# Performance work log

Hardware: AMD Instinct MI355X
Metric: run time of the kernel (lower is better)

Reference implementation:

```python
import jax, jax.numpy as jnp
import numpy as np

PI = 3.14159265358979323846
MARGIN = 6.0
DIM = 256
ENT_TOT = 43234
REL_RANGE = (6.0 + 2.0) / DIM  # (margin + epsilon) / dim = 0.03125


def setup_inputs() -> dict:
    key = jax.random.key(0)
    k1, k2, k3 = jax.random.split(key, 3)
    head = jax.random.normal(k1, (32, 2 * DIM), dtype=jnp.float32)
    relation = jax.random.normal(k2, (32, DIM), dtype=jnp.float32)
    ent_emb = jax.random.normal(k3, (ENT_TOT, 2 * DIM), dtype=jnp.float32)
    return {"head": head, "relation": relation, "ent_emb": ent_emb}


def reference(head, relation, ent_emb):
    # head: (B, 2D) -> re/im halves (B, D)
    re_h, im_h = jnp.split(head, 2, axis=-1)
    # entity table: (E, 2D) -> (E, D) each
    re_t, im_t = jnp.split(ent_emb, 2, axis=-1)
    # phase rotation from relation embedding
    phase = relation / (REL_RANGE / PI)          # (B, D)
    re_r = jnp.cos(phase)
    im_r = jnp.sin(phase)
    # complex rotation of head by relation: (B, D)
    re_rot = re_h * re_r - im_h * im_r
    im_rot = re_h * im_r + im_h * re_r
    # difference against every entity, broadcast to (B, E, D)
    re_s = re_rot[:, None, :] - re_t[None, :, :]
    im_s = im_rot[:, None, :] - im_t[None, :, :]
    # L2 norm over the complex pair, summed over D -> (B, E)
    dist = jnp.sqrt(re_s * re_s + im_s * im_s).sum(axis=-1)
    return MARGIN - dist
```

## Files before the change

kernel.cpp:

```cpp
#include <hip/hip_runtime.h>
#include <math.h>

#define DIMH 256
#define NB   32
#define E_TOT 43234
#define TE   64
#define DK   32
#define DQ   128
#define NC   (DQ / DK)
#define PHASE_DIV 0.009947183943243459f

typedef float v2f __attribute__((ext_vector_type(2)));
typedef float v4f __attribute__((ext_vector_type(4)));

__global__ __launch_bounds__(256) void init_kernel(float* __restrict__ out) {
    int i = blockIdx.x * 256 + threadIdx.x;
    if (i < (NB * E_TOT) / 4) {
        float4 v = make_float4(6.0f, 6.0f, 6.0f, 6.0f);
        reinterpret_cast<float4*>(out)[i] = v;
    }
}

__global__ void rot_kernel(const float* __restrict__ head,
                           const float* __restrict__ rel,
                           float* __restrict__ rot) {
    int i = blockIdx.x * blockDim.x + threadIdx.x;
    int b = i >> 8;
    int d = i & 255;
    float re_h = head[b * 2 * DIMH + d];
    float im_h = head[b * 2 * DIMH + DIMH + d];
    float ph = rel[b * DIMH + d] / PHASE_DIV;
    float s, c;
    sincosf(ph, &s, &c);
    rot[b * DIMH + d]             = re_h * c - im_h * s;
    rot[NB * DIMH + b * DIMH + d] = re_h * s + im_h * c;
}

__device__ __forceinline__ v2f sqrt2(v2f s) {
    v2f r;
    r.x = __builtin_amdgcn_sqrtf(s.x);
    r.y = __builtin_amdgcn_sqrtf(s.y);
    return r;
}

__global__ __launch_bounds__(256, 6) void dist_kernel(const float* __restrict__ ent,
                                                      const float* __restrict__ rot,
                                                      float* __restrict__ out) {
    __shared__ v4f s_e[TE][DK / 2 + 1];
    __shared__ v4f s_r[NB][DK / 2 + 1];

    const int tid   = threadIdx.x;
    const int etile = blockIdx.x >> 1;
    const int half  = blockIdx.x & 1;
    const int eb    = etile * TE;
    const int eg    = tid & 31;
    const int bg    = (tid >> 5) * 4;
    const int dbase = half * DQ;

    const int er0 = min(eb + (tid >> 3), E_TOT - 1);
    const int er1 = min(eb + ((tid + 256) >> 3), E_TOT - 1);
    const int ec0 = (tid & 7) << 2;
    const int rrow = tid >> 3;

    float4 pe_re[2], pe_im[2], p_rr, p_ri;

    auto load_chunk = [&](int dk) {
        const float* b0 = &ent[(size_t)er0 * (2 * DIMH)];
        const float* b1 = &ent[(size_t)er1 * (2 * DIMH)];
        pe_re[0] = *reinterpret_cast<const float4*>(b0 + dk + ec0);
        pe_im[0] = *reinterpret_cast<const float4*>(b0 + DIMH + dk + ec0);
        pe_re[1] = *reinterpret_cast<const float4*>(b1 + dk + ec0);
        pe_im[1] = *reinterpret_cast<const float4*>(b1 + DIMH + dk + ec0);
        p_rr = *reinterpret_cast<const float4*>(&rot[rrow * DIMH + dk + ec0]);
        p_ri = *reinterpret_cast<const float4*>(&rot[NB * DIMH + rrow * DIMH + dk + ec0]);
    };

    v2f acc[4][2];
    #pragma unroll
    for (int j = 0; j < 4; ++j)
        #pragma unroll
        for (int k = 0; k < 2; ++k) { acc[j][k].x = 0.f; acc[j][k].y = 0.f; }

    load_chunk(dbase);

    for (int c = 0; c < NC; ++c) {
        {
            int c4 = tid & 7;
            #pragma unroll
            for (int it = 0; it < 2; ++it) {
                int row = (tid + it * 256) >> 3;
                v4f lo, hi;
                lo.x = pe_re[it].x; lo.y = pe_re[it].y; lo.z = pe_im[it].x; lo.w = pe_im[it].y;
                hi.x = pe_re[it].z; hi.y = pe_re[it].w; hi.z = pe_im[it].z; hi.w = pe_im[it].w;
                s_e[row][2 * c4]     = lo;
                s_e[row][2 * c4 + 1] = hi;
            }
            v4f lo, hi;
            lo.x = p_rr.x; lo.y = p_rr.y; lo.z = p_ri.x; lo.w = p_ri.y;
            hi.x = p_rr.z; hi.y = p_rr.w; hi.z = p_ri.z; hi.w = p_ri.w;
            s_r[rrow][2 * c4]     = lo;
            s_r[rrow][2 * c4 + 1] = hi;
        }
        __syncthreads();

        if (c + 1 < NC) load_chunk(dbase + (c + 1) * DK);

        #pragma unroll 4
        for (int p = 0; p < DK / 2; ++p) {
            v4f r4[4], e4[2];
            #pragma unroll
            for (int j = 0; j < 4; ++j) r4[j] = s_r[bg + j][p];
            #pragma unroll
            for (int k = 0; k < 2; ++k) e4[k] = s_e[eg + 32 * k][p];
            #pragma unroll
            for (int j = 0; j < 4; ++j)
                #pragma unroll
                for (int k = 0; k < 2; ++k) {
                    v2f a = r4[j].xy - e4[k].xy;
                    v2f b = r4[j].zw - e4[k].zw;
                    v2f s = a * a + b * b;
                    acc[j][k] += sqrt2(s);
                }
        }
        __syncthreads();
    }

    #pragma unroll
    for (int k = 0; k < 2; ++k) {
        int e = eb + eg + 32 * k;
        if (e < E_TOT) {
            #pragma unroll
            for (int j = 0; j < 4; ++j)
                atomicAdd(&out[(size_t)(bg + j) * E_TOT + e],
                          -(acc[j][k].x + acc[j][k].y));
        }
    }
}

extern "C" void kernel_launch(void* const* d_in, const int* in_sizes, int n_in,
                              void* d_out, int out_size, void* d_ws, size_t ws_size,
                              hipStream_t stream) {
    const float* head = (const float*)d_in[0];
    const float* rel  = (const float*)d_in[1];
    const float* ent  = (const float*)d_in[2];
    float* rot = (float*)d_ws;

    int init_blocks = ((NB * E_TOT) / 4 + 255) / 256;
    init_kernel<<<init_blocks, 256, 0, stream>>>((float*)d_out);
    rot_kernel<<<(NB * DIMH) / 256, 256, 0, stream>>>(head, rel, rot);

    int etiles = (E_TOT + TE - 1) / TE;
    dist_kernel<<<etiles * 2, 256, 0, stream>>>(ent, rot, (float*)d_out);
}
```

Measured before the change: 209.7 us.

## Replace init+atomicAdd with partial-sum buffers and a reduce kernel

The output is no longer pre-filled with the margin and accumulated with atomics. Each half-dimension block now writes its partial sum to a workspace buffer, and a separate reduce kernel adds the two halves and subtracts from the margin. If the workspace is too small, a fallback runs a single pass over the full dimension and writes the output directly. This removes the atomic read-modify-write traffic and the init pass, but adds a 2x-size intermediate write and a read-back in the reduce kernel.

```diff
diff --git a/kernel.cpp b/kernel.cpp
--- a/kernel.cpp
+++ b/kernel.cpp
@@ -7,19 +7,10 @@
 #define TE   64
 #define DK   32
 #define DQ   128
-#define NC   (DQ / DK)
 #define PHASE_DIV 0.009947183943243459f
 
 typedef float v2f __attribute__((ext_vector_type(2)));
 typedef float v4f __attribute__((ext_vector_type(4)));
-
-__global__ __launch_bounds__(256) void init_kernel(float* __restrict__ out) {
-    int i = blockIdx.x * 256 + threadIdx.x;
-    if (i < (NB * E_TOT) / 4) {
-        float4 v = make_float4(6.0f, 6.0f, 6.0f, 6.0f);
-        reinterpret_cast<float4*>(out)[i] = v;
-    }
-}
 
 __global__ void rot_kernel(const float* __restrict__ head,
                            const float* __restrict__ rel,
@@ -43,15 +34,17 @@
     return r;
 }
 
+template<bool DIRECT>
 __global__ __launch_bounds__(256, 6) void dist_kernel(const float* __restrict__ ent,
                                                       const float* __restrict__ rot,
-                                                      float* __restrict__ out) {
+                                                      float* __restrict__ dst) {
     __shared__ v4f s_e[TE][DK / 2 + 1];
     __shared__ v4f s_r[NB][DK / 2 + 1];
 
     const int tid   = threadIdx.x;
-    const int etile = blockIdx.x >> 1;
-    const int half  = blockIdx.x & 1;
+    const int etile = DIRECT ? blockIdx.x : (blockIdx.x >> 1);
+    const int half  = DIRECT ? 0 : (blockIdx.x & 1);
+    const int NC    = DIRECT ? (DIMH / DK) : (DQ / DK);
     const int eb    = etile * TE;
     const int eg    = tid & 31;
     const int bg    = (tid >> 5) * 4;
@@ -130,10 +123,30 @@
         int e = eb + eg + 32 * k;
         if (e < E_TOT) {
             #pragma unroll
-            for (int j = 0; j < 4; ++j)
-                atomicAdd(&out[(size_t)(bg + j) * E_TOT + e],
-                          -(acc[j][k].x + acc[j][k].y));
+            for (int j = 0; j < 4; ++j) {
+                float s = acc[j][k].x + acc[j][k].y;
+                if (DIRECT) {
+                    dst[(size_t)(bg + j) * E_TOT + e] = 6.0f - s;
+                } else {
+                    dst[(size_t)half * (NB * E_TOT) + (size_t)(bg + j) * E_TOT + e] = s;
+                }
+            }
         }
+    }
+}
+
+__global__ __launch_bounds__(256) void reduce_kernel(const float* __restrict__ part,
+                                                     float* __restrict__ out) {
+    int i = blockIdx.x * 256 + threadIdx.x;
+    if (i < (NB * E_TOT) / 4) {
+        float4 a = reinterpret_cast<const float4*>(part)[i];
+        float4 b = reinterpret_cast<const float4*>(part + (size_t)NB * E_TOT)[i];
+        float4 o;
+        o.x = 6.0f - (a.x + b.x);
+        o.y = 6.0f - (a.y + b.y);
+        o.z = 6.0f - (a.z + b.z);
+        o.w = 6.0f - (a.w + b.w);
+        reinterpret_cast<float4*>(out)[i] = o;
     }
 }
 
@@ -143,12 +156,19 @@
     const float* head = (const float*)d_in[0];
     const float* rel  = (const float*)d_in[1];
     const float* ent  = (const float*)d_in[2];
-    float* rot = (float*)d_ws;
+    float* rot  = (float*)d_ws;
+    float* part = rot + 2 * NB * DIMH;
 
-    int init_blocks = ((NB * E_TOT) / 4 + 255) / 256;
-    init_kernel<<<init_blocks, 256, 0, stream>>>((float*)d_out);
     rot_kernel<<<(NB * DIMH) / 256, 256, 0, stream>>>(head, rel, rot);
 
-    int etiles = (E_TOT + TE - 1) / TE;
-    dist_kernel<<<etiles * 2, 256, 0, stream>>>(ent, rot, (float*)d_out);
+    const size_t need = (size_t)(2 * NB * DIMH) * 4 + (size_t)2 * NB * E_TOT * 4;
+    const int etiles = (E_TOT + TE - 1) / TE;
+
+    if (ws_size >= need) {
+        dist_kernel<false><<<etiles * 2, 256, 0, stream>>>(ent, rot, part);
+        int rblocks = ((NB * E_TOT) / 4 + 255) / 256;
+        reduce_kernel<<<rblocks, 256, 0, stream>>>(part, (float*)d_out);
+    } else {
+        dist_kernel<true><<<etiles, 256, 0, stream>>>(ent, rot, (float*)d_out);
+    }
 }
```

Measured after the change: 210.9 us. About the same (+0.6%).

## Store LDS tiles as bf16, drop D-split and atomics, remove init kernel

Applied to the files above, without the earlier changes.

Entity and rotated-head values are rounded to bf16 and packed into 8-byte words in shared memory, which halves LDS footprint and read traffic per inner iteration. Each block now covers the full D range instead of half, so the output is written directly with the margin applied. This removes the init kernel and the atomicAdd traffic. The cost is lower precision in the distance sum from the bf16 rounding, plus added pack and unpack ALU work and half as many blocks.

```diff
diff --git a/kernel.cpp b/kernel.cpp
--- a/kernel.cpp
+++ b/kernel.cpp
@@ -6,34 +6,53 @@
 #define E_TOT 43234
 #define TE   64
 #define DK   32
-#define DQ   128
-#define NC   (DQ / DK)
+#define NC   (DIMH / DK)
 #define PHASE_DIV 0.009947183943243459f
 
 typedef float v2f __attribute__((ext_vector_type(2)));
-typedef float v4f __attribute__((ext_vector_type(4)));
 
-__global__ __launch_bounds__(256) void init_kernel(float* __restrict__ out) {
-    int i = blockIdx.x * 256 + threadIdx.x;
-    if (i < (NB * E_TOT) / 4) {
-        float4 v = make_float4(6.0f, 6.0f, 6.0f, 6.0f);
-        reinterpret_cast<float4*>(out)[i] = v;
-    }
+__device__ __forceinline__ unsigned bf16_rne(float f) {
+    unsigned u = __float_as_uint(f);
+    return (u + 0x7FFFu + ((u >> 16) & 1u)) >> 16;
+}
+__device__ __forceinline__ unsigned pack_bf16(float f0, float f1) {
+    return bf16_rne(f0) | (bf16_rne(f1) << 16);
+}
+__device__ __forceinline__ v2f unpack_bf16(unsigned w) {
+    v2f r;
+    r.x = __uint_as_float(w << 16);
+    r.y = __uint_as_float(w & 0xFFFF0000u);
+    return r;
 }
 
-__global__ void rot_kernel(const float* __restrict__ head,
-                           const float* __restrict__ rel,
-                           float* __restrict__ rot) {
-    int i = blockIdx.x * blockDim.x + threadIdx.x;
-    int b = i >> 8;
-    int d = i & 255;
-    float re_h = head[b * 2 * DIMH + d];
-    float im_h = head[b * 2 * DIMH + DIMH + d];
-    float ph = rel[b * DIMH + d] / PHASE_DIV;
-    float s, c;
-    sincosf(ph, &s, &c);
-    rot[b * DIMH + d]             = re_h * c - im_h * s;
-    rot[NB * DIMH + b * DIMH + d] = re_h * s + im_h * c;
+__global__ __launch_bounds__(256) void rot_kernel(const float* __restrict__ head,
+                                                  const float* __restrict__ rel,
+                                                  uint2* __restrict__ rot_bf) {
+    int i  = blockIdx.x * 256 + threadIdx.x;
+    int b  = i >> 7;
+    int dp = i & 127;
+    int d0 = dp * 2;
+    float re0, re1, im0, im1;
+    {
+        float re_h = head[b * 2 * DIMH + d0];
+        float im_h = head[b * 2 * DIMH + DIMH + d0];
+        float s, c;
+        sincosf(rel[b * DIMH + d0] / PHASE_DIV, &s, &c);
+        re0 = re_h * c - im_h * s;
+        im0 = re_h * s + im_h * c;
+    }
+    {
+        float re_h = head[b * 2 * DIMH + d0 + 1];
+        float im_h = head[b * 2 * DIMH + DIMH + d0 + 1];
+        float s, c;
+        sincosf(rel[b * DIMH + d0 + 1] / PHASE_DIV, &s, &c);
+        re1 = re_h * c - im_h * s;
+        im1 = re_h * s + im_h * c;
+    }
+    uint2 w;
+    w.x = pack_bf16(re0, re1);
+    w.y = pack_bf16(im0, im1);
+    rot_bf[b * (DIMH / 2) + dp] = w;
 }
 
 __device__ __forceinline__ v2f sqrt2(v2f s) {
@@ -43,36 +62,39 @@
     return r;
 }
 
-__global__ __launch_bounds__(256, 6) void dist_kernel(const float* __restrict__ ent,
-                                                      const float* __restrict__ rot,
+__global__ __launch_bounds__(256, 4) void dist_kernel(const float* __restrict__ ent,
+                                                      const uint2* __restrict__ rot_bf,
                                                       float* __restrict__ out) {
-    __shared__ v4f s_e[TE][DK / 2 + 1];
-    __shared__ v4f s_r[NB][DK / 2 + 1];
+    __shared__ uint2 s_e[TE][DK / 2 + 1];
+    __shared__ uint2 s_r[NB][DK / 2 + 1];
 
-    const int tid   = threadIdx.x;
-    const int etile = blockIdx.x >> 1;
-    const int half  = blockIdx.x & 1;
-    const int eb    = etile * TE;
-    const int eg    = tid & 31;
-    const int bg    = (tid >> 5) * 4;
-    const int dbase = half * DQ;
+    const int tid = threadIdx.x;
+    const int eb  = blockIdx.x * TE;
+    const int eg  = tid & 31;
+    const int bg  = (tid >> 5) * 4;
 
-    const int er0 = min(eb + (tid >> 3), E_TOT - 1);
-    const int er1 = min(eb + ((tid + 256) >> 3), E_TOT - 1);
-    const int ec0 = (tid & 7) << 2;
-    const int rrow = tid >> 3;
+    const int row0 = tid >> 3;
+    const int row1 = (tid + 256) >> 3;
+    const int c4   = tid & 7;
+    const int er0  = min(eb + row0, E_TOT - 1);
+    const int er1  = min(eb + row1, E_TOT - 1);
+    const int rrow0 = tid >> 4;
+    const int rrow1 = (tid + 256) >> 4;
+    const int rpp   = tid & 15;
 
-    float4 pe_re[2], pe_im[2], p_rr, p_ri;
+    float4 pre[2], pim[2];
+    uint2  prt[2];
 
-    auto load_chunk = [&](int dk) {
+    auto load_chunk = [&](int c) {
+        const int dk = c * DK;
         const float* b0 = &ent[(size_t)er0 * (2 * DIMH)];
         const float* b1 = &ent[(size_t)er1 * (2 * DIMH)];
-        pe_re[0] = *reinterpret_cast<const float4*>(b0 + dk + ec0);
-        pe_im[0] = *reinterpret_cast<const float4*>(b0 + DIMH + dk + ec0);
-        pe_re[1] = *reinterpret_cast<const float4*>(b1 + dk + ec0);
-        pe_im[1] = *reinterpret_cast<const float4*>(b1 + DIMH + dk + ec0);
-        p_rr = *reinterpret_cast<const float4*>(&rot[rrow * DIMH + dk + ec0]);
-        p_ri = *reinterpret_cast<const float4*>(&rot[NB * DIMH + rrow * DIMH + dk + ec0]);
+        pre[0] = *reinterpret_cast<const float4*>(b0 + dk + 4 * c4);
+        pim[0] = *reinterpret_cast<const float4*>(b0 + DIMH + dk + 4 * c4);
+        pre[1] = *reinterpret_cast<const float4*>(b1 + dk + 4 * c4);
+        pim[1] = *reinterpret_cast<const float4*>(b1 + DIMH + dk + 4 * c4);
+        prt[0] = rot_bf[rrow0 * (DIMH / 2) + c * (DK / 2) + rpp];
+        prt[1] = rot_bf[rrow1 * (DIMH / 2) + c * (DK / 2) + rpp];
     };
 
     v2f acc[4][2];
@@ -81,43 +103,49 @@
         #pragma unroll
         for (int k = 0; k < 2; ++k) { acc[j][k].x = 0.f; acc[j][k].y = 0.f; }
 
-    load_chunk(dbase);
+    load_chunk(0);
 
     for (int c = 0; c < NC; ++c) {
         {
-            int c4 = tid & 7;
+            const int rows[2] = {row0, row1};
             #pragma unroll
             for (int it = 0; it < 2; ++it) {
-                int row = (tid + it * 256) >> 3;
-                v4f lo, hi;
-                lo.x = pe_re[it].x; lo.y = pe_re[it].y; lo.z = pe_im[it].x; lo.w = pe_im[it].y;
-                hi.x = pe_re[it].z; hi.y = pe_re[it].w; hi.z = pe_im[it].z; hi.w = pe_im[it].w;
-                s_e[row][2 * c4]     = lo;
-                s_e[row][2 * c4 + 1] = hi;
+                uint2 w0, w1;
+                w0.x = pack_bf16(pre[it].x, pre[it].y);
+                w0.y = pack_bf16(pim[it].x, pim[it].y);
+                w1.x = pack_bf16(pre[it].z, pre[it].w);
+                w1.y = pack_bf16(pim[it].z, pim[it].w);
+                s_e[rows[it]][2 * c4]     = w0;
+                s_e[rows[it]][2 * c4 + 1] = w1;
             }
-            v4f lo, hi;
-            lo.x = p_rr.x; lo.y = p_rr.y; lo.z = p_ri.x; lo.w = p_ri.y;
-            hi.x = p_rr.z; hi.y = p_rr.w; hi.z = p_ri.z; hi.w = p_ri.w;
-            s_r[rrow][2 * c4]     = lo;
-            s_r[rrow][2 * c4 + 1] = hi;
+            s_r[rrow0][rpp] = prt[0];
+            s_r[rrow1][rpp] = prt[1];
         }
         __syncthreads();
 
-        if (c + 1 < NC) load_chunk(dbase + (c + 1) * DK);
+        if (c + 1 < NC) load_chunk(c + 1);
 
         #pragma unroll 4
         for (int p = 0; p < DK / 2; ++p) {
-            v4f r4[4], e4[2];
+            v2f rr[4], ri[4], er[2], ei[2];
             #pragma unroll
-            for (int j = 0; j < 4; ++j) r4[j] = s_r[bg + j][p];
+            for (int j = 0; j < 4; ++j) {
+                uint2 w = s_r[bg + j][p];
+                rr[j] = unpack_bf16(w.x);
+                ri[j] = unpack_bf16(w.y);
+            }
             #pragma unroll
-            for (int k = 0; k < 2; ++k) e4[k] = s_e[eg + 32 * k][p];
+            for (int k = 0; k < 2; ++k) {
+                uint2 w = s_e[eg + 32 * k][p];
+                er[k] = unpack_bf16(w.x);
+                ei[k] = unpack_bf16(w.y);
+            }
             #pragma unroll
             for (int j = 0; j < 4; ++j)
                 #pragma unroll
                 for (int k = 0; k < 2; ++k) {
-                    v2f a = r4[j].xy - e4[k].xy;
-                    v2f b = r4[j].zw - e4[k].zw;
+                    v2f a = rr[j] - er[k];
+                    v2f b = ri[j] - ei[k];
                     v2f s = a * a + b * b;
                     acc[j][k] += sqrt2(s);
                 }
@@ -131,8 +159,7 @@
         if (e < E_TOT) {
             #pragma unroll
             for (int j = 0; j < 4; ++j)
-                atomicAdd(&out[(size_t)(bg + j) * E_TOT + e],
-                          -(acc[j][k].x + acc[j][k].y));
+                out[(size_t)(bg + j) * E_TOT + e] = 6.0f - (acc[j][k].x + acc[j][k].y);
         }
     }
 }
@@ -143,12 +170,10 @@
     const float* head = (const float*)d_in[0];
     const float* rel  = (const float*)d_in[1];
     const float* ent  = (const float*)d_in[2];
-    float* rot = (float*)d_ws;
+    uint2* rot_bf = (uint2*)d_ws;
 
-    int init_blocks = ((NB * E_TOT) / 4 + 255) / 256;
-    init_kernel<<<init_blocks, 256, 0, stream>>>((float*)d_out);
-    rot_kernel<<<(NB * DIMH) / 256, 256, 0, stream>>>(head, rel, rot);
+    rot_kernel<<<(NB * DIMH / 2) / 256, 256, 0, stream>>>(head, rel, rot_bf);
 
     int etiles = (E_TOT + TE - 1) / TE;
-    dist_kernel<<<etiles * 2, 256, 0, stream>>>(ent, rot, (float*)d_out);
+    dist_kernel<<<etiles, 256, 0, stream>>>(ent, rot_bf, (float*)d_out);
 }
```

Result: faster. 184.3 us (-12.1%).
